# Optimization experiments

Hardware: AMD Instinct MI355X
Metric: run time of the kernel (lower is better)

The kernel has to match this reference:

```python
import jax, jax.numpy as jnp
import numpy as np

B, C, T = 8, 128, 8192
SIGMA_MIN = 1e-6

def setup_inputs() -> dict:
    key = jax.random.key(0)
    ks = jax.random.split(key, 9)
    x1 = jax.random.normal(ks[0], (B, C, T), dtype=jnp.float32)
    mu = jax.random.normal(ks[1], (B, C, T), dtype=jnp.float32)
    style = jax.random.normal(ks[2], (B, 192), dtype=jnp.float32)
    t_sample = jax.random.uniform(ks[3], (B, 1, 1), dtype=jnp.float32)
    z = jax.random.normal(ks[4], (B, C, T), dtype=jnp.float32)
    W = jax.random.normal(ks[5], (C, C), dtype=jnp.float32) * (1.0 / np.sqrt(C))
    b_lin = jax.random.normal(ks[6], (C,), dtype=jnp.float32) * 0.01
    prompt_lens = jax.random.randint(ks[7], (B,), 64, T // 4)
    x_lens = jax.random.randint(ks[8], (B,), T // 2, T)
    return {"x1": x1, "mu": mu, "style": style, "t_sample": t_sample, "z": z,
            "W": W, "b_lin": b_lin, "x_lens": x_lens, "prompt_lens": prompt_lens}

def reference(x1, mu, style, t_sample, z, W, b_lin, x_lens, prompt_lens):
    # x1, z: [B, C, T]; t_sample: [B, 1, 1]
    sigma = SIGMA_MIN
    Bb, Cc, Tt = x1.shape
    tpos = jnp.arange(Tt)
    pmask = tpos[None, :] < prompt_lens[:, None]            # [B, T] prompt region
    # flow-matching interpolation
    y = (1.0 - (1.0 - sigma) * t_sample) * z + t_sample * x1
    u = x1 - (1.0 - sigma) * z
    # zero out prompt region of y (prompt copy tensor is unused by the mock estimator)
    y = jnp.where(pmask[:, None, :], 0.0, y)
    # mock estimator: per-timestep Linear over channels
    out = jnp.einsum('bct,dc->bdt', y, W) + b_lin[None, :, None]
    # per-sample MSE over [prompt_lens, x_lens) across all channels, then mean over batch
    lmask = (~pmask) & (tpos[None, :] < x_lens[:, None])     # [B, T]
    diff2 = jnp.square(out - u) * lmask[:, None, :]
    counts = (Cc * jnp.sum(lmask, axis=1)).astype(x1.dtype)  # [B]
    loss = jnp.mean(jnp.sum(diff2, axis=(1, 2)) / counts)
    return loss, out + (1.0 - sigma) * z
```

## Files before the change

kernel.cpp:

```cpp
#include <hip/hip_runtime.h>
#include <hip/hip_bf16.h>

#define BB    8
#define CC    128
#define TLEN  8192
#define TT    32
#define TILES 4
#define TSPAN (TT * TILES)
#define NB    (BB * (TLEN / TSPAN))

typedef __attribute__((ext_vector_type(8))) short short8;
typedef __attribute__((ext_vector_type(4))) float f32x4;

__device__ __forceinline__ short f2bf(float f) {
    union { float f; unsigned u; } v; v.f = f;
    return (short)((v.u + 0x7FFFu + ((v.u >> 16) & 1u)) >> 16);
}
__device__ __forceinline__ int swzY(int t, int c) {
    return c ^ (((t ^ (t >> 3)) & 15) << 3);
}
__device__ __forceinline__ int sfz(int c) {
    return ((c & 3) << 3) | (((c >> 2) & 1) << 2);
}

#define VMWAIT(N) asm volatile("s_waitcnt vmcnt(" #N ")" ::: "memory")

__device__ __forceinline__ void bar_lgkm() {
    asm volatile("s_waitcnt lgkmcnt(0)" ::: "memory");
    __builtin_amdgcn_s_barrier();
}

typedef __attribute__((address_space(1))) const unsigned GU;
typedef __attribute__((address_space(3))) unsigned LU;
__device__ __forceinline__ void glds16(const float* g, const float* l) {
    __builtin_amdgcn_global_load_lds((GU*)g, (LU*)l, 16, 0, 0);
}

__global__ __launch_bounds__(512, 4)
void cfm_fused(const float* __restrict__ x1, const float* __restrict__ tsm,
               const float* __restrict__ z, const float* __restrict__ W,
               const float* __restrict__ blin, const int* __restrict__ xlens,
               const int* __restrict__ plens, float* __restrict__ out)
{
    __shared__ float xf[2][CC * TT];
    __shared__ float zf[2][CC * TT];
    __shared__ short ybf[TT][CC];
    __shared__ float red[8];

    const int bi    = blockIdx.x;
    const int b     = bi & 7;
    const int tbase = (bi >> 3) * TSPAN;

    const int tid  = threadIdx.x;
    const int lane = tid & 63;
    const int wid  = tid >> 6;
    const int r15  = lane & 15;
    const int q4   = lane >> 4;

    const float ts  = tsm[b];
    const int   pl  = plens[b];
    const int   xl  = xlens[b];
    const float oms = 0.999999f;
    const float cz  = 1.0f - oms * ts;
    const float cx  = ts;

    short8 af[4];
    {
        const int row = wid * 16 + r15;
        #pragma unroll
        for (int ks = 0; ks < 4; ++ks) {
            const float4 w0 = *reinterpret_cast<const float4*>(W + row * CC + ks * 32 + q4 * 8);
            const float4 w1 = *reinterpret_cast<const float4*>(W + row * CC + ks * 32 + q4 * 8 + 4);
            short8 a;
            a[0] = f2bf(w0.x); a[1] = f2bf(w0.y); a[2] = f2bf(w0.z); a[3] = f2bf(w0.w);
            a[4] = f2bf(w1.x); a[5] = f2bf(w1.y); a[6] = f2bf(w1.z); a[7] = f2bf(w1.w);
            af[ks] = a;
        }
    }
    float bl[4];
    #pragma unroll
    for (int rr = 0; rr < 4; ++rr) bl[rr] = blin[wid * 16 + q4 * 4 + rr];

    const int cl  = lane >> 3;
    const int tsw = ((lane & 7) * 4) ^ sfz(cl);
    const size_t gB = (size_t)b * CC * TLEN;
    const int ca = wid * 16, cb = ca + 8;

    #define STAGE(buf, t0k) do {                                              \
        glds16(x1 + gB + (size_t)(ca + cl) * TLEN + (t0k) + tsw, &xf[buf][ca * TT]); \
        glds16(x1 + gB + (size_t)(cb + cl) * TLEN + (t0k) + tsw, &xf[buf][cb * TT]); \
        glds16(z  + gB + (size_t)(ca + cl) * TLEN + (t0k) + tsw, &zf[buf][ca * TT]); \
        glds16(z  + gB + (size_t)(cb + cl) * TLEN + (t0k) + tsw, &zf[buf][cb * TT]); \
    } while (0)

    const int rc  = tid >> 2;
    const int tg8 = (tid & 3) * 8;
    const int fidx = (rc * TT + tg8) ^ sfz(rc);

    #define REPACK(buf, t0k) do {                                             \
        const f32x4 xa = *reinterpret_cast<const f32x4*>(&xf[buf][fidx]);     \
        const f32x4 xb = *reinterpret_cast<const f32x4*>(&xf[buf][fidx ^ 4]); \
        const f32x4 za = *reinterpret_cast<const f32x4*>(&zf[buf][fidx]);     \
        const f32x4 zb = *reinterpret_cast<const f32x4*>(&zf[buf][fidx ^ 4]); \
        _Pragma("unroll")                                                     \
        for (int j = 0; j < 4; ++j) {                                         \
            const int t0j = tg8 + j, t1j = tg8 + 4 + j;                       \
            const float y0 = ((t0k) + t0j < pl) ? 0.0f : cz * za[j] + cx * xa[j]; \
            const float y1 = ((t0k) + t1j < pl) ? 0.0f : cz * zb[j] + cx * xb[j]; \
            ybf[t0j][swzY(t0j, rc)] = f2bf(y0);                               \
            ybf[t1j][swzY(t1j, rc)] = f2bf(y1);                               \
        }                                                                     \
    } while (0)

    float lsum = 0.0f;
    #define COMPUTE(buf, t0k) do {                                            \
        f32x4 acc[2];                                                         \
        acc[0] = (f32x4){0,0,0,0}; acc[1] = (f32x4){0,0,0,0};                 \
        _Pragma("unroll")                                                     \
        for (int ks = 0; ks < 4; ++ks) {                                      \
            _Pragma("unroll")                                                 \
            for (int tt = 0; tt < 2; ++tt) {                                  \
                const int tr = tt * 16 + r15;                                 \
                const short8 ya = *reinterpret_cast<const short8*>(           \
                    &ybf[tr][swzY(tr, ks * 32 + q4 * 8)]);                    \
                acc[tt] = __builtin_amdgcn_mfma_f32_16x16x32_bf16(af[ks], ya, acc[tt], 0, 0, 0); \
            }                                                                 \
        }                                                                     \
        _Pragma("unroll")                                                     \
        for (int rr = 0; rr < 4; ++rr) {                                      \
            const int d = wid * 16 + q4 * 4 + rr;                             \
            float* orow = out + 1 + (size_t)(b * CC + d) * TLEN + (t0k);      \
            _Pragma("unroll")                                                 \
            for (int tt = 0; tt < 2; ++tt) {                                  \
                const int tl = tt * 16 + r15;                                 \
                const int fi = (d * TT + tl) ^ sfz(d);                        \
                const float zfv = zf[buf][fi];                                \
                const float xfv = xf[buf][fi];                                \
                const float ov  = acc[tt][rr] + bl[rr];                       \
                const float o2  = ov + oms * zfv;                             \
                orow[tl] = o2;                                                \
                const int tgl = (t0k) + tl;                                   \
                if ((tgl >= pl) & (tgl < xl)) { const float df = o2 - xfv; lsum += df * df; } \
            }                                                                 \
        }                                                                     \
    } while (0)

    STAGE(0, tbase);
    STAGE(1, tbase + TT);

    VMWAIT(4);  __builtin_amdgcn_sched_barrier(0); bar_lgkm();
    REPACK(0, tbase);                       bar_lgkm();
    COMPUTE(0, tbase);                      bar_lgkm();
    STAGE(0, tbase + 2 * TT);

    VMWAIT(12); __builtin_amdgcn_sched_barrier(0); bar_lgkm();
    REPACK(1, tbase + TT);                  bar_lgkm();
    COMPUTE(1, tbase + TT);                 bar_lgkm();
    STAGE(1, tbase + 3 * TT);

    VMWAIT(12); __builtin_amdgcn_sched_barrier(0); bar_lgkm();
    REPACK(0, tbase + 2 * TT);              bar_lgkm();
    COMPUTE(0, tbase + 2 * TT);             bar_lgkm();

    VMWAIT(8);  __builtin_amdgcn_sched_barrier(0); bar_lgkm();
    REPACK(1, tbase + 3 * TT);              bar_lgkm();
    COMPUTE(1, tbase + 3 * TT);

    #pragma unroll
    for (int off = 32; off >= 1; off >>= 1) lsum += __shfl_down(lsum, off);
    if (lane == 0) red[wid] = lsum;
    __syncthreads();
    if (tid == 0) {
        float s = 0.0f;
        #pragma unroll
        for (int w = 0; w < 8; ++w) s += red[w];
        atomicAdd(out, s / (1024.0f * (float)(xl - pl)));
    }
}

extern "C" void kernel_launch(void* const* d_in, const int* in_sizes, int n_in,
                              void* d_out, int out_size, void* d_ws, size_t ws_size,
                              hipStream_t stream) {
    const float* x1    = (const float*)d_in[0];
    const float* tsm   = (const float*)d_in[3];
    const float* z     = (const float*)d_in[4];
    const float* W     = (const float*)d_in[5];
    const float* blin  = (const float*)d_in[6];
    const int*   xlens = (const int*)d_in[7];
    const int*   plens = (const int*)d_in[8];
    float* out = (float*)d_out;

    hipMemsetAsync(out, 0, sizeof(float), stream);
    cfm_fused<<<NB, 512, 0, stream>>>(x1, tsm, z, W, blin, xlens, plens, out);
}
```

Before: 30.45 us.

## Load x1 into registers and pack z/x1 as bf16 for the epilogue

x1 is now read straight into registers with inline global_load_dwordx4 instead of being staged through LDS, so only z is double-buffered in shared memory. During repack, z and x1 are packed as bf16 pairs into a single LDS array that the epilogue reads with one load per element. The next tile's loads are issued before the MFMA compute, and a barrier after compute is dropped. This cuts LDS footprint and traffic. The cost is that the output and loss now use bf16-rounded z and x1, which may break accuracy tolerance. The inline-asm loads also depend on hand-tuned vmcnt waits for correctness.

```diff
diff --git a/kernel.cpp b/kernel.cpp
--- a/kernel.cpp
+++ b/kernel.cpp
@@ -5,8 +5,7 @@
 #define CC    128
 #define TLEN  8192
 #define TT    32
-#define TILES 4
-#define TSPAN (TT * TILES)
+#define TSPAN 128
 #define NB    (BB * (TLEN / TSPAN))
 
 typedef __attribute__((ext_vector_type(8))) short short8;
@@ -16,6 +15,10 @@
     union { float f; unsigned u; } v; v.f = f;
     return (short)((v.u + 0x7FFFu + ((v.u >> 16) & 1u)) >> 16);
 }
+__device__ __forceinline__ float bf2f(unsigned short h) {
+    union { unsigned u; float f; } v; v.u = ((unsigned)h) << 16;
+    return v.f;
+}
 __device__ __forceinline__ int swzY(int t, int c) {
     return c ^ (((t ^ (t >> 3)) & 15) << 3);
 }
@@ -24,6 +27,7 @@
 }
 
 #define VMWAIT(N) asm volatile("s_waitcnt vmcnt(" #N ")" ::: "memory")
+#define SB0 __builtin_amdgcn_sched_barrier(0)
 
 __device__ __forceinline__ void bar_lgkm() {
     asm volatile("s_waitcnt lgkmcnt(0)" ::: "memory");
@@ -34,6 +38,12 @@
 typedef __attribute__((address_space(3))) unsigned LU;
 __device__ __forceinline__ void glds16(const float* g, const float* l) {
     __builtin_amdgcn_global_load_lds((GU*)g, (LU*)l, 16, 0, 0);
+}
+__device__ __forceinline__ f32x4 gload(const float* base, unsigned byteoff) {
+    f32x4 r;
+    asm volatile("global_load_dwordx4 %0, %1, %2"
+                 : "=v"(r) : "v"(byteoff), "s"(base));
+    return r;
 }
 
 __global__ __launch_bounds__(512, 4)
@@ -42,14 +52,14 @@
                const float* __restrict__ blin, const int* __restrict__ xlens,
                const int* __restrict__ plens, float* __restrict__ out)
 {
-    __shared__ float xf[2][CC * TT];
-    __shared__ float zf[2][CC * TT];
-    __shared__ short ybf[TT][CC];
-    __shared__ float red[8];
-
-    const int bi    = blockIdx.x;
-    const int b     = bi & 7;
-    const int tbase = (bi >> 3) * TSPAN;
+    __shared__ float    zfb[2][CC * TT];
+    __shared__ short    ybf[TT][CC];
+    __shared__ unsigned zxpk[CC * TT];
+    __shared__ float    red[8];
+
+    const int bi = blockIdx.x;
+    const int b  = bi & 7;
+    const int tb = (bi >> 3) * TSPAN;
 
     const int tid  = threadIdx.x;
     const int lane = tid & 63;
@@ -63,6 +73,7 @@
     const float oms = 0.999999f;
     const float cz  = 1.0f - oms * ts;
     const float cx  = ts;
+    const size_t gB = (size_t)b * CC * TLEN;
 
     short8 af[4];
     {
@@ -77,43 +88,46 @@
             af[ks] = a;
         }
     }
-    float bl[4];
-    #pragma unroll
-    for (int rr = 0; rr < 4; ++rr) bl[rr] = blin[wid * 16 + q4 * 4 + rr];
+    f32x4 blv = *reinterpret_cast<const f32x4*>(blin + wid * 16 + q4 * 4);
+    asm volatile("" :: "v"(blv));
 
     const int cl  = lane >> 3;
     const int tsw = ((lane & 7) * 4) ^ sfz(cl);
-    const size_t gB = (size_t)b * CC * TLEN;
-    const int ca = wid * 16, cb = ca + 8;
-
-    #define STAGE(buf, t0k) do {                                              \
-        glds16(x1 + gB + (size_t)(ca + cl) * TLEN + (t0k) + tsw, &xf[buf][ca * TT]); \
-        glds16(x1 + gB + (size_t)(cb + cl) * TLEN + (t0k) + tsw, &xf[buf][cb * TT]); \
-        glds16(z  + gB + (size_t)(ca + cl) * TLEN + (t0k) + tsw, &zf[buf][ca * TT]); \
-        glds16(z  + gB + (size_t)(cb + cl) * TLEN + (t0k) + tsw, &zf[buf][cb * TT]); \
+    const int ca  = wid * 16, cb = ca + 8;
+    #define STAGEZ(buf, t0k) do {                                             \
+        glds16(z + gB + (size_t)(ca + cl) * TLEN + (t0k) + tsw, &zfb[buf][ca * TT]); \
+        glds16(z + gB + (size_t)(cb + cl) * TLEN + (t0k) + tsw, &zfb[buf][cb * TT]); \
     } while (0)
 
     const int rc  = tid >> 2;
-    const int tg8 = (tid & 3) * 8;
-    const int fidx = (rc * TT + tg8) ^ sfz(rc);
-
-    #define REPACK(buf, t0k) do {                                             \
-        const f32x4 xa = *reinterpret_cast<const f32x4*>(&xf[buf][fidx]);     \
-        const f32x4 xb = *reinterpret_cast<const f32x4*>(&xf[buf][fidx ^ 4]); \
-        const f32x4 za = *reinterpret_cast<const f32x4*>(&zf[buf][fidx]);     \
-        const f32x4 zb = *reinterpret_cast<const f32x4*>(&zf[buf][fidx ^ 4]); \
+    const int t8  = (tid & 3) * 8;
+    const int fz  = sfz(rc);
+    const unsigned xoff = (unsigned)((gB + (size_t)rc * TLEN) * 4);
+    #define XLOAD(xr, t0k) do {                                               \
+        xr[0] = gload(x1, xoff + ((t0k) + t8) * 4u);                          \
+        xr[1] = gload(x1, xoff + ((t0k) + t8 + 4) * 4u);                      \
+    } while (0)
+
+    #define REPACK(buf, t0k, xr) do {                                         \
+        const int idx = (rc * TT + t8) ^ fz;                                  \
+        const f32x4 za = *reinterpret_cast<const f32x4*>(&zfb[buf][idx]);     \
+        const f32x4 zb = *reinterpret_cast<const f32x4*>(&zfb[buf][idx ^ 4]); \
         _Pragma("unroll")                                                     \
         for (int j = 0; j < 4; ++j) {                                         \
-            const int t0j = tg8 + j, t1j = tg8 + 4 + j;                       \
-            const float y0 = ((t0k) + t0j < pl) ? 0.0f : cz * za[j] + cx * xa[j]; \
-            const float y1 = ((t0k) + t1j < pl) ? 0.0f : cz * zb[j] + cx * xb[j]; \
-            ybf[t0j][swzY(t0j, rc)] = f2bf(y0);                               \
-            ybf[t1j][swzY(t1j, rc)] = f2bf(y1);                               \
+            const int ta = t8 + j, tb2 = t8 + 4 + j;                          \
+            const float y0 = ((t0k) + ta  < pl) ? 0.0f : cz * za[j] + cx * xr[0][j]; \
+            const float y1 = ((t0k) + tb2 < pl) ? 0.0f : cz * zb[j] + cx * xr[1][j]; \
+            ybf[ta][swzY(ta, rc)]   = f2bf(y0);                               \
+            ybf[tb2][swzY(tb2, rc)] = f2bf(y1);                               \
+            zxpk[idx + j]       = ((unsigned)(unsigned short)f2bf(xr[0][j]) << 16) \
+                                | (unsigned)(unsigned short)f2bf(za[j]);      \
+            zxpk[(idx ^ 4) + j] = ((unsigned)(unsigned short)f2bf(xr[1][j]) << 16) \
+                                | (unsigned)(unsigned short)f2bf(zb[j]);      \
         }                                                                     \
     } while (0)
 
     float lsum = 0.0f;
-    #define COMPUTE(buf, t0k) do {                                            \
+    #define COMPUTE(t0k) do {                                                 \
         f32x4 acc[2];                                                         \
         acc[0] = (f32x4){0,0,0,0}; acc[1] = (f32x4){0,0,0,0};                 \
         _Pragma("unroll")                                                     \
@@ -130,41 +144,46 @@
         for (int rr = 0; rr < 4; ++rr) {                                      \
             const int d = wid * 16 + q4 * 4 + rr;                             \
             float* orow = out + 1 + (size_t)(b * CC + d) * TLEN + (t0k);      \
+            const int fd = sfz(d);                                            \
             _Pragma("unroll")                                                 \
             for (int tt = 0; tt < 2; ++tt) {                                  \
                 const int tl = tt * 16 + r15;                                 \
-                const int fi = (d * TT + tl) ^ sfz(d);                        \
-                const float zfv = zf[buf][fi];                                \
-                const float xfv = xf[buf][fi];                                \
-                const float ov  = acc[tt][rr] + bl[rr];                       \
-                const float o2  = ov + oms * zfv;                             \
+                const unsigned p = zxpk[(d * TT + tl) ^ fd];                  \
+                const float zv = bf2f((unsigned short)(p & 0xFFFFu));         \
+                const float xv = bf2f((unsigned short)(p >> 16));             \
+                const float o2 = acc[tt][rr] + blv[rr] + oms * zv;            \
                 orow[tl] = o2;                                                \
-                const int tgl = (t0k) + tl;                                   \
-                if ((tgl >= pl) & (tgl < xl)) { const float df = o2 - xfv; lsum += df * df; } \
+                const int tg = (t0k) + tl;                                    \
+                if ((tg >= pl) & (tg < xl)) { const float df = o2 - xv; lsum += df * df; } \
             }                                                                 \
         }                                                                     \
     } while (0)
 
-    STAGE(0, tbase);
-    STAGE(1, tbase + TT);
-
-    VMWAIT(4);  __builtin_amdgcn_sched_barrier(0); bar_lgkm();
-    REPACK(0, tbase);                       bar_lgkm();
-    COMPUTE(0, tbase);                      bar_lgkm();
-    STAGE(0, tbase + 2 * TT);
-
-    VMWAIT(12); __builtin_amdgcn_sched_barrier(0); bar_lgkm();
-    REPACK(1, tbase + TT);                  bar_lgkm();
-    COMPUTE(1, tbase + TT);                 bar_lgkm();
-    STAGE(1, tbase + 3 * TT);
-
-    VMWAIT(12); __builtin_amdgcn_sched_barrier(0); bar_lgkm();
-    REPACK(0, tbase + 2 * TT);              bar_lgkm();
-    COMPUTE(0, tbase + 2 * TT);             bar_lgkm();
-
-    VMWAIT(8);  __builtin_amdgcn_sched_barrier(0); bar_lgkm();
-    REPACK(1, tbase + 3 * TT);              bar_lgkm();
-    COMPUTE(1, tbase + 3 * TT);
+    f32x4 x0r[2], x1r[2];
+    STAGEZ(0, tb);          XLOAD(x0r, tb);          SB0;
+    STAGEZ(1, tb + TT);     XLOAD(x1r, tb + TT);     SB0;
+
+    VMWAIT(4); SB0; bar_lgkm();
+    REPACK(0, tb, x0r);
+    bar_lgkm();
+    STAGEZ(0, tb + 2 * TT); XLOAD(x0r, tb + 2 * TT); SB0;
+    COMPUTE(tb);
+
+    VMWAIT(12); SB0; bar_lgkm();
+    REPACK(1, tb + TT, x1r);
+    bar_lgkm();
+    STAGEZ(1, tb + 3 * TT); XLOAD(x1r, tb + 3 * TT); SB0;
+    COMPUTE(tb + TT);
+
+    VMWAIT(20); SB0; bar_lgkm();
+    REPACK(0, tb + 2 * TT, x0r);
+    bar_lgkm();
+    COMPUTE(tb + 2 * TT);
+
+    VMWAIT(16); SB0; bar_lgkm();
+    REPACK(1, tb + 3 * TT, x1r);
+    bar_lgkm();
+    COMPUTE(tb + 3 * TT);
 
     #pragma unroll
     for (int off = 32; off >= 1; off >>= 1) lsum += __shfl_down(lsum, off);
```

New measurement: 30.86 us. No clear change (+1.3%).
